# Performance work log

Measured on AMD Instinct MI355X. Metric: run time of the kernel, lower is better.

## Reference

```python
import jax, jax.numpy as jnp
import numpy as np

B, N, M = 1, 16384, 16384
K_NEIGH = 16
KERNEL_SIZE = 15
C_IN, C_OUT = 64, 128
RADIUS = 1.0


def setup_inputs() -> dict:
    key = jax.random.key(0)
    k1, k2, k3, k4, k5 = jax.random.split(key, 5)
    query_points = jax.random.normal(k1, (B, N, 3), dtype=jnp.float32)
    support_points = query_points  # typical KPConv: support == query
    neighbor_idx = jax.random.randint(k2, (B, N, K_NEIGH), 0, M)
    features = jax.random.normal(k3, (B, M, C_IN), dtype=jnp.float32)
    weights = jax.random.normal(k4, (KERNEL_SIZE, C_IN, C_OUT), dtype=jnp.float32) * 0.005
    # kernel points: random unit directions scaled to radius, first fixed at center
    kp = jax.random.normal(k5, (KERNEL_SIZE, 3), dtype=jnp.float32)
    kp = kp / jnp.linalg.norm(kp, axis=1, keepdims=True) * RADIUS
    kernel_points = kp.at[0].set(jnp.zeros(3, dtype=jnp.float32))
    return {
        "query_points": query_points,
        "support_points": support_points,
        "neighbor_idx": neighbor_idx,
        "features": features,
        "weights": weights,
        "kernel_points": kernel_points,
    }


def reference(query_points, support_points, neighbor_idx, features, weights, kernel_points):
    # gather neighbor features and coords: (B,N,k,C), (B,N,k,3)
    gather = jax.vmap(lambda arr, idx: arr[idx])
    neighbor_feats = gather(features, neighbor_idx)
    neighbor_coords = gather(support_points, neighbor_idx)
    # relative coords to query: (B,N,k,3)
    rel = neighbor_coords - query_points[:, :, None, :]
    # distance to each kernel point: (B,N,k,P)
    diff = rel[:, :, :, None, :] - kernel_points[None, None, None, :, :]
    dists = jnp.linalg.norm(diff, axis=-1)
    # linear influence
    infl = jnp.clip(1.0 - dists / RADIUS, 0.0)
    # weighted sum over neighbors -> (B,N,P,C) without materializing (B,N,k,P,C)
    aggregated = jnp.einsum('bnkp,bnkc->bnpc', infl, neighbor_feats)
    # per-kernel-point matmul -> (B,N,C_out)
    return jnp.einsum('bnpc,pco->bno', aggregated, weights)
```

## Files before the change

### kernel.cpp

```cpp
#include <hip/hip_runtime.h>

typedef __attribute__((ext_vector_type(8))) short bf16x8;
typedef __attribute__((ext_vector_type(4))) float f32x4;

constexpr int N_PTS = 16384;
constexpr int KN = 16;
constexpr int P  = 15;
constexpr int CI = 64;
constexpr int CO = 128;
constexpr int QB = 32;
constexpr int KTOT   = P * CI;
constexpr int KSTEPS = KTOT / 32;
constexpr int APITCH = KTOT + 8;
constexpr int PF = 4;

static __device__ __forceinline__ unsigned short f2bf(float f) {
    unsigned u = __float_as_uint(f);
    u = (u + 0x7fffu + ((u >> 16) & 1u)) >> 16;
    return (unsigned short)u;
}
#define BFLO(u) __uint_as_float((unsigned)(u) << 16)
#define BFHI(u) __uint_as_float((unsigned)(u) & 0xFFFF0000u)

__global__ __launch_bounds__(256) void prep_w(const float* __restrict__ W,
                                              unsigned short* __restrict__ WB) {
    const int t = blockIdx.x * 256 + threadIdx.x;
    const int l  = t & 63;
    const int kb = (t >> 9) * 32 + ((l >> 4) * 8);
    const int o  = ((t >> 6) & 7) * 16 + (l & 15);
    unsigned short v[8];
    #pragma unroll
    for (int j = 0; j < 8; ++j) v[j] = f2bf(W[(size_t)(kb + j) * CO + o]);
    uint4 q;
    q.x = v[0] | ((unsigned)v[1] << 16);
    q.y = v[2] | ((unsigned)v[3] << 16);
    q.z = v[4] | ((unsigned)v[5] << 16);
    q.w = v[6] | ((unsigned)v[7] << 16);
    *(uint4*)&WB[(size_t)t * 8] = q;
}

__global__ __launch_bounds__(512, 4) void kpconv_main(
    const float* __restrict__ query,
    const float* __restrict__ support,
    const int*   __restrict__ nidx,
    const float* __restrict__ feats,
    const unsigned short* __restrict__ WB,
    const float* __restrict__ kp,
    float* __restrict__ out)
{
    __shared__ float sKp[P][3];
    __shared__ unsigned short sIdxS[QB][KN];
    __shared__ int sCnt[QB];
    __shared__ unsigned char sKlist[QB][KN];
    __shared__ __align__(16) unsigned short sInflB[QB][KN][16];
    __shared__ __align__(16) unsigned short sAgg[QB][APITCH];

    const int t  = threadIdx.x;
    const int n0 = blockIdx.x * QB;
    const int w  = t >> 6, l = t & 63;

    if (t < P * 3) ((float*)sKp)[t] = kp[t];
    if (t < QB) sCnt[t] = 0;
    __syncthreads();

    {
        const int pt = t >> 4, k = t & 15;
        const int n = n0 + pt;
        const int idx = nidx[n * KN + k];
        sIdxS[pt][k] = (unsigned short)idx;
        const float rx = support[idx * 3 + 0] - query[n * 3 + 0];
        const float ry = support[idx * 3 + 1] - query[n * 3 + 1];
        const float rz = support[idx * 3 + 2] - query[n * 3 + 2];
        unsigned short h[16];
        float mx = 0.0f;
        #pragma unroll
        for (int p = 0; p < P; ++p) {
            const float dx = rx - sKp[p][0];
            const float dy = ry - sKp[p][1];
            const float dz = rz - sKp[p][2];
            const float infl = fmaxf(1.0f - sqrtf(dx*dx + dy*dy + dz*dz), 0.0f);
            mx = fmaxf(mx, infl);
            h[p] = f2bf(infl);
        }
        h[15] = 0;
        uint4 u0, u1;
        u0.x = h[0] | ((unsigned)h[1] << 16);   u0.y = h[2] | ((unsigned)h[3] << 16);
        u0.z = h[4] | ((unsigned)h[5] << 16);   u0.w = h[6] | ((unsigned)h[7] << 16);
        u1.x = h[8] | ((unsigned)h[9] << 16);   u1.y = h[10] | ((unsigned)h[11] << 16);
        u1.z = h[12] | ((unsigned)h[13] << 16); u1.w = h[14];
        *(uint4*)&sInflB[pt][k][0] = u0;
        *(uint4*)&sInflB[pt][k][8] = u1;
        if (mx > 0.0f) {
            const int slot = atomicAdd(&sCnt[pt], 1);
            sKlist[pt][slot] = (unsigned char)k;
        }
    }
    __syncthreads();

    {
        const int pt = t >> 4;
        const int c  = (t & 15) * 4;
        const int nk = sCnt[pt];
        f32x4 A0={0,0,0,0},A1={0,0,0,0},A2={0,0,0,0},A3={0,0,0,0},A4={0,0,0,0};
        f32x4 A5={0,0,0,0},A6={0,0,0,0},A7={0,0,0,0},A8={0,0,0,0},A9={0,0,0,0};
        f32x4 A10={0,0,0,0},A11={0,0,0,0},A12={0,0,0,0},A13={0,0,0,0},A14={0,0,0,0};
        for (int i = 0; i < nk; ++i) {
            const int k   = sKlist[pt][i];
            const int idx = sIdxS[pt][k];
            const f32x4 fv = *(const f32x4*)&feats[(size_t)idx * CI + c];
            const uint4 u0 = *(const uint4*)&sInflB[pt][k][0];
            const uint4 u1 = *(const uint4*)&sInflB[pt][k][8];
            A0  += BFLO(u0.x) * fv;  A1  += BFHI(u0.x) * fv;
            A2  += BFLO(u0.y) * fv;  A3  += BFHI(u0.y) * fv;
            A4  += BFLO(u0.z) * fv;  A5  += BFHI(u0.z) * fv;
            A6  += BFLO(u0.w) * fv;  A7  += BFHI(u0.w) * fv;
            A8  += BFLO(u1.x) * fv;  A9  += BFHI(u1.x) * fv;
            A10 += BFLO(u1.y) * fv;  A11 += BFHI(u1.y) * fv;
            A12 += BFLO(u1.z) * fv;  A13 += BFHI(u1.z) * fv;
            A14 += BFLO(u1.w) * fv;
        }
        #define STORE_P(p, Ap)                                                  \
            do {                                                                \
                uint2 wv;                                                       \
                wv.x = f2bf(Ap.x) | ((unsigned)f2bf(Ap.y) << 16);               \
                wv.y = f2bf(Ap.z) | ((unsigned)f2bf(Ap.w) << 16);               \
                *(uint2*)&sAgg[pt][(p) * CI + c] = wv;                          \
            } while (0)
        STORE_P(0, A0);  STORE_P(1, A1);  STORE_P(2, A2);  STORE_P(3, A3);
        STORE_P(4, A4);  STORE_P(5, A5);  STORE_P(6, A6);  STORE_P(7, A7);
        STORE_P(8, A8);  STORE_P(9, A9);  STORE_P(10, A10); STORE_P(11, A11);
        STORE_P(12, A12); STORE_P(13, A13); STORE_P(14, A14);
        #undef STORE_P
    }
    __syncthreads();

    {
        f32x4 c0 = {0.f, 0.f, 0.f, 0.f};
        f32x4 c1 = {0.f, 0.f, 0.f, 0.f};
        const int kq = (l >> 4) * 8;
        const unsigned short* a0 = &sAgg[l & 15][kq];
        const unsigned short* a1 = &sAgg[16 + (l & 15)][kq];
        const unsigned short* wb = &WB[(size_t)(w * 64 + l) * 8];
        bf16x8 pb[PF];
        #pragma unroll
        for (int s = 0; s < PF; ++s) pb[s] = *(const bf16x8*)&wb[(size_t)s * 4096];
        #pragma unroll
        for (int s = 0; s < KSTEPS; ++s) {
            const bf16x8 av0 = *(const bf16x8*)&a0[s * 32];
            const bf16x8 av1 = *(const bf16x8*)&a1[s * 32];
            const bf16x8 bv = pb[s & (PF - 1)];
            c0 = __builtin_amdgcn_mfma_f32_16x16x32_bf16(av0, bv, c0, 0, 0, 0);
            c1 = __builtin_amdgcn_mfma_f32_16x16x32_bf16(av1, bv, c1, 0, 0, 0);
            if (s + PF < KSTEPS) pb[s & (PF - 1)] = *(const bf16x8*)&wb[(size_t)(s + PF) * 4096];
        }
        const int o0 = w * 16 + (l & 15);
        const int r0 = n0 + (l >> 4) * 4;
        #pragma unroll
        for (int r = 0; r < 4; ++r) {
            out[(size_t)(r0 + r) * CO + o0]      = c0[r];
            out[(size_t)(r0 + 16 + r) * CO + o0] = c1[r];
        }
    }
}

extern "C" void kernel_launch(void* const* d_in, const int* in_sizes, int n_in,
                              void* d_out, int out_size, void* d_ws, size_t ws_size,
                              hipStream_t stream) {
    const float* query   = (const float*)d_in[0];
    const float* support = (const float*)d_in[1];
    const int*   nidx    = (const int*)d_in[2];
    const float* feats   = (const float*)d_in[3];
    const float* W       = (const float*)d_in[4];
    const float* kp      = (const float*)d_in[5];
    float* out = (float*)d_out;
    unsigned short* WB = (unsigned short*)d_ws;

    hipLaunchKernelGGL(prep_w, dim3(60), dim3(256), 0, stream, W, WB);
    hipLaunchKernelGGL(kpconv_main, dim3(N_PTS / QB), dim3(512), 0, stream,
                       query, support, nidx, feats, WB, kp, out);
}
```

Baseline: 86.24 us.

## Prefetch all input tensors into L2/MALL in the weight-prep kernel

The weight-prep kernel grows to 512 blocks and also streams nidx, query, support and the full feature table with coalesced 16-byte loads, XOR-reducing the values into a workspace sink so the loads are not eliminated. The goal is to warm the cache so the main kernel's random feature gathers and index loads hit cache instead of HBM. The cost is an extra full read of about 5.6 MB of inputs in the prep launch. The net effect depends on whether that data survives in L2 or the last-level cache until the main kernel runs.

Result: no change. 87.91 us (+1.9%).

```diff
diff --git a/kernel.cpp b/kernel.cpp
--- a/kernel.cpp
+++ b/kernel.cpp
@@ -13,6 +13,7 @@
 constexpr int KSTEPS = KTOT / 32;
 constexpr int APITCH = KTOT + 8;
 constexpr int PF = 4;
+constexpr size_t TOUCH_OFF = 262144;
 
 static __device__ __forceinline__ unsigned short f2bf(float f) {
     unsigned u = __float_as_uint(f);
@@ -22,21 +23,45 @@
 #define BFLO(u) __uint_as_float((unsigned)(u) << 16)
 #define BFHI(u) __uint_as_float((unsigned)(u) & 0xFFFF0000u)
 
-__global__ __launch_bounds__(256) void prep_w(const float* __restrict__ W,
-                                              unsigned short* __restrict__ WB) {
+__global__ __launch_bounds__(256) void prep(const float* __restrict__ W,
+                                            const float* __restrict__ feats,
+                                            const int*   __restrict__ nidx,
+                                            const float* __restrict__ query,
+                                            const float* __restrict__ support,
+                                            unsigned short* __restrict__ WB,
+                                            unsigned* __restrict__ touchOut) {
     const int t = blockIdx.x * 256 + threadIdx.x;
-    const int l  = t & 63;
-    const int kb = (t >> 9) * 32 + ((l >> 4) * 8);
-    const int o  = ((t >> 6) & 7) * 16 + (l & 15);
-    unsigned short v[8];
+
+    unsigned acc = 0;
     #pragma unroll
-    for (int j = 0; j < 8; ++j) v[j] = f2bf(W[(size_t)(kb + j) * CO + o]);
-    uint4 q;
-    q.x = v[0] | ((unsigned)v[1] << 16);
-    q.y = v[2] | ((unsigned)v[3] << 16);
-    q.z = v[4] | ((unsigned)v[5] << 16);
-    q.w = v[6] | ((unsigned)v[7] << 16);
-    *(uint4*)&WB[(size_t)t * 8] = q;
+    for (int j = 0; j < 3; ++j) {
+        const int c = j * 131072 + t;
+        if (c < 352256) {
+            const uint4* p;
+            if (c < 65536)       p = (const uint4*)nidx    + c;
+            else if (c < 77824)  p = (const uint4*)query   + (c - 65536);
+            else if (c < 90112)  p = (const uint4*)support + (c - 77824);
+            else                 p = (const uint4*)feats   + (c - 90112);
+            const uint4 v = *p;
+            acc ^= v.x ^ v.y ^ v.z ^ v.w;
+        }
+    }
+    touchOut[t] = acc;
+
+    if (t < 15360) {
+        const int l  = t & 63;
+        const int kb = (t >> 9) * 32 + ((l >> 4) * 8);
+        const int o  = ((t >> 6) & 7) * 16 + (l & 15);
+        unsigned short v[8];
+        #pragma unroll
+        for (int j = 0; j < 8; ++j) v[j] = f2bf(W[(size_t)(kb + j) * CO + o]);
+        uint4 q;
+        q.x = v[0] | ((unsigned)v[1] << 16);
+        q.y = v[2] | ((unsigned)v[3] << 16);
+        q.z = v[4] | ((unsigned)v[5] << 16);
+        q.w = v[6] | ((unsigned)v[7] << 16);
+        *(uint4*)&WB[(size_t)t * 8] = q;
+    }
 }
 
 __global__ __launch_bounds__(512, 4) void kpconv_main(
@@ -174,8 +199,10 @@
     const float* kp      = (const float*)d_in[5];
     float* out = (float*)d_out;
     unsigned short* WB = (unsigned short*)d_ws;
-
-    hipLaunchKernelGGL(prep_w, dim3(60), dim3(256), 0, stream, W, WB);
+    unsigned* touchOut = (unsigned*)((char*)d_ws + TOUCH_OFF);
+
+    hipLaunchKernelGGL(prep, dim3(512), dim3(256), 0, stream,
+                       W, feats, nidx, query, support, WB, touchOut);
     hipLaunchKernelGGL(kpconv_main, dim3(N_PTS / QB), dim3(512), 0, stream,
                        query, support, nidx, feats, WB, kp, out);
 }
```
